# Optimization experiments

Hardware: AMD Instinct MI355X
Metric: run time of the kernel (lower is better)

## Reference

```python
import jax, jax.numpy as jnp
import numpy as np

T_STEPS = 64      # AR order p
MAX_T = 65536     # trajectory length
BATCH = 256       # number of sampled trajectories
STD = 0.3


def setup_inputs() -> dict:
    key = jax.random.key(0)
    k1, k2, k3 = jax.random.split(key, 3)
    raw = jax.random.normal(k1, (T_STEPS,), dtype=jnp.float32)
    # torch init: params / sum(|params|)
    params = raw / jnp.sum(jnp.abs(raw))
    bias = jax.random.uniform(k2, (1,), dtype=jnp.float32)
    noise = jax.random.normal(k3, (BATCH, MAX_T), dtype=jnp.float32)
    return {"params": params, "bias": bias, "noise": noise}


def _ar_means(params, bias, length):
    """AR(p) recurrence: mean_i = sum_k params[k] * x[i-1-k] + bias, x init = 0.
    State holds the last p values, most-recent-first (matches the reversed
    indexing inputs[i-1 : i-p-1 : -1] in the torch code)."""
    p = params.shape[0]

    def step(state, _):
        new = jnp.dot(state, params) + bias[0]
        state = jnp.concatenate([new[None], state[:-1]])
        return state, new

    init = jnp.zeros((p,), dtype=params.dtype)
    _, means = jax.lax.scan(step, init, None, length=length)
    return means  # [length]


def reference(params, bias, noise):
    # means of the Normal over the trajectory (deterministic, shared by batch)
    means = _ar_means(params, bias, noise.shape[1])  # [T]
    # reparameterized sample: actions = mean + std * eps, eps ~ N(0, 1)
    actions = means[None, :] + jnp.asarray(STD, noise.dtype) * noise  # [B, T]
    return actions
```

## Files before the change

kernel.cpp:

```cpp
#include <hip/hip_runtime.h>

#define T_LEN   65536
#define BATCH   256
#define P       64
#define K1_LEN  8192
#define K1_THREADS 256
#define W_TILE  1024
#define BCHUNK  8
#define VOFF    65536
#define V3OFF   (VOFF + 80)

typedef float f4 __attribute__((ext_vector_type(4)));


__global__ __launch_bounds__(K1_THREADS, 1) void ar_k1(const float* __restrict__ params,
                                                       float* __restrict__ R) {
    __shared__ __align__(16) float Rl[K1_LEN];
    __shared__ float p[128];
    __shared__ float Wp[64][4];
    __shared__ __align__(16) float Vs[68];
    __shared__ __align__(16) float tailb[192];
    __shared__ float t3[128];
    const int tid = threadIdx.x;
    if (tid < 128) p[tid] = (tid < P) ? params[tid] : 0.f;
    __syncthreads();

    if (tid < 64) {
        float z = 0.f;
        const float pk = p[tid];
        for (int t = 0; t < 64; ++t) {
            float y  = __shfl(z, 0) + 1.0f;
            float zn = __shfl_down(z, 1);
            if (tid == 63) zn = 0.f;
            z = fmaf(pk, y, zn);
            if (tid == 0) Rl[t] = y;
        }
    }
    __syncthreads();

    for (int L = 64; L <= K1_LEN; L <<= 1) {
        const bool last = (L == K1_LEN);
        {
            const int j = tid >> 2, c = tid & 3;
            const int mbase = c << 4;
            float w = 0.f;
            #pragma unroll
            for (int mm = 0; mm < 16; ++mm) {
                const int m = mbase + mm;
                w = fmaf(p[m + j], Rl[L - 1 - m], w);
            }
            Wp[j][c] = w;
        }
        __syncthreads();
        if (tid <= P) {
            const float wj  = (tid < P)
                ? (Wp[tid][0] + Wp[tid][1] + Wp[tid][2] + Wp[tid][3]) : 0.f;
            const float wm1 = (tid >= 1)
                ? (Wp[tid-1][0] + Wp[tid-1][1] + Wp[tid-1][2] + Wp[tid-1][3]) : 0.f;
            Vs[tid] = wj - wm1;
        }
        __syncthreads();
        if (tid < P) {
            const int tau = tid;
            float acc = Rl[tau];
            #pragma unroll
            for (int i = 0; i < P; ++i) {
                const int idx = (tau - i) > 0 ? (tau - i) : 0;
                const float v = (i <= tau) ? Vs[i] : 0.f;
                acc = fmaf(v, Rl[idx], acc);
            }
            if (last) R[L + tau] = acc; else Rl[L + tau] = acc;
        }
        {
            const f4* __restrict__ Rl4 = reinterpret_cast<const f4*>(Rl);
            f4* __restrict__ Rl4w = reinterpret_cast<f4*>(Rl);
            f4* __restrict__ Rg4  = reinterpret_cast<f4*>(R);
            const f4* __restrict__ V4 = reinterpret_cast<const f4*>(Vs);
            const int nq = (L - 64) >> 2;
            #pragma unroll 1
            for (int q = tid; q < nq; q += K1_THREADS) {
                f4 w4[17];
                #pragma unroll
                for (int j = 0; j < 17; ++j) w4[j] = Rl4[q + j];
                float a0 = w4[16].x, a1 = w4[16].y, a2 = w4[16].z, a3 = w4[16].w;
                #pragma unroll
                for (int g = 0; g < 16; ++g) {
                    const f4 v  = V4[g];
                    const f4 hi = w4[16 - g];
                    const f4 lo = w4[15 - g];
                    a0 = fmaf(v.x, hi.x, a0); a1 = fmaf(v.x, hi.y, a1);
                    a2 = fmaf(v.x, hi.z, a2); a3 = fmaf(v.x, hi.w, a3);
                    a0 = fmaf(v.y, lo.w, a0); a1 = fmaf(v.y, hi.x, a1);
                    a2 = fmaf(v.y, hi.y, a2); a3 = fmaf(v.y, hi.z, a3);
                    a0 = fmaf(v.z, lo.z, a0); a1 = fmaf(v.z, lo.w, a1);
                    a2 = fmaf(v.z, hi.x, a2); a3 = fmaf(v.z, hi.y, a3);
                    a0 = fmaf(v.w, lo.y, a0); a1 = fmaf(v.w, lo.z, a1);
                    a2 = fmaf(v.w, lo.w, a2); a3 = fmaf(v.w, hi.x, a3);
                }
                const float v64 = Vs[64];
                a0 = fmaf(v64, w4[0].x, a0); a1 = fmaf(v64, w4[0].y, a1);
                a2 = fmaf(v64, w4[0].z, a2); a3 = fmaf(v64, w4[0].w, a3);
                f4 o; o.x = a0; o.y = a1; o.z = a2; o.w = a3;
                if (last) {
                    Rg4[((L + 64) >> 2) + q] = o;
                    if (q >= 1984) reinterpret_cast<f4*>(tailb)[q - 1984] = o;
                } else {
                    Rl4w[((L + 64) >> 2) + q] = o;
                }
            }
        }
        __syncthreads();
    }

    {
        const int j = tid >> 2, c = tid & 3, mbase = c << 4;
        float w = 0.f;
        #pragma unroll
        for (int mm = 0; mm < 16; ++mm) {
            const int m = mbase + mm;
            w = fmaf(p[m + j], tailb[191 - m], w);
        }
        Wp[j][c] = w;
    }
    __syncthreads();
    if (tid <= P) {
        const float wj  = (tid < P)
            ? (Wp[tid][0] + Wp[tid][1] + Wp[tid][2] + Wp[tid][3]) : 0.f;
        const float wm1 = (tid >= 1)
            ? (Wp[tid-1][0] + Wp[tid-1][1] + Wp[tid-1][2] + Wp[tid-1][3]) : 0.f;
        const float v = wj - wm1;
        Vs[tid] = v;
        R[VOFF + tid] = v;
    }
    __syncthreads();
    if (tid < 128) {
        float acc = tailb[64 + tid];
        #pragma unroll
        for (int i = 0; i <= P; ++i)
            acc = fmaf(Vs[i], tailb[64 + tid - i], acc);
        t3[tid] = acc;
    }
    __syncthreads();
    {
        const int j = tid >> 2, c = tid & 3, mbase = c << 4;
        float w = 0.f;
        #pragma unroll
        for (int mm = 0; mm < 16; ++mm) {
            const int m = mbase + mm;
            w = fmaf(p[m + j], t3[127 - m], w);
        }
        Wp[j][c] = w;
    }
    __syncthreads();
    if (tid <= P) {
        const float wj  = (tid < P)
            ? (Wp[tid][0] + Wp[tid][1] + Wp[tid][2] + Wp[tid][3]) : 0.f;
        const float wm1 = (tid >= 1)
            ? (Wp[tid-1][0] + Wp[tid-1][1] + Wp[tid-1][2] + Wp[tid-1][3]) : 0.f;
        R[V3OFF + tid] = wj - wm1;
    }

    for (int j = tid; j < K1_LEN / 4; j += K1_THREADS)
        reinterpret_cast<f4*>(R)[j] = reinterpret_cast<const f4*>(Rl)[j];
}

__global__ __launch_bounds__(256) void ar_out_fused(const float* __restrict__ R,
                                                    const float* __restrict__ bias,
                                                    const float* __restrict__ noise,
                                                    float* __restrict__ out) {
    __shared__ __align__(16) float Rt[W_TILE];
    __shared__ float winA[W_TILE + 64];
    __shared__ float winB[W_TILE + 128];
    __shared__ float V2l[72], V3l[72];
    const int tid  = threadIdx.x;
    const int tile = blockIdx.x & 63;
    const int bc   = blockIdx.x >> 6;
    const int t0   = tile * W_TILE;
    const float b  = bias[0];

    if (tid < 65)       V2l[tid] = R[VOFF + tid];
    else if (tid < 130) V3l[tid - 65] = R[V3OFF + (tid - 65)];

    f4 rt;
    if (t0 < 16384) {
        const f4 r = reinterpret_cast<const f4*>(R)[(t0 >> 2) + tid];
        rt.x = b * r.x; rt.y = b * r.y; rt.z = b * r.z; rt.w = b * r.w;
    } else if (t0 < 32768) {
        const int u0 = t0 - 16384;
        for (int k = tid; k < W_TILE + 64; k += 256) {
            const int u = u0 - 64 + k;
            winA[k] = (u >= 0) ? R[u] : 0.f;
        }
        __syncthreads();
        for (int j = tid; j < W_TILE; j += 256) {
            float acc = winA[64 + j];
            #pragma unroll
            for (int i = 0; i <= P; ++i)
                acc = fmaf(V2l[i], winA[64 + j - i], acc);
            Rt[j] = b * acc;
        }
        __syncthreads();
        rt = reinterpret_cast<const f4*>(Rt)[tid];
    } else {
        const int tau0 = t0 - 32768;
        const int s0   = tau0 - 64;
        if (tau0 >= 16384) {
            const int wb0 = s0 - 16448;
            for (int k = tid; k < W_TILE + 128; k += 256) {
                const int u = wb0 + k;
                winB[k] = (u >= 0) ? R[u] : 0.f;
            }
        }
        __syncthreads();
        for (int k = tid; k < W_TILE + 64; k += 256) {
            const int u = s0 + k;
            float v;
            if (u < 0) {
                v = 0.f;
            } else if (u < 16384) {
                v = R[u];
            } else {
                float a = winB[k + 64];
                #pragma unroll
                for (int i = 0; i <= P; ++i)
                    a = fmaf(V2l[i], winB[k + 64 - i], a);
                v = a;
            }
            winA[k] = v;
        }
        __syncthreads();
        for (int j = tid; j < W_TILE; j += 256) {
            float acc = winA[64 + j];
            #pragma unroll
            for (int i = 0; i <= P; ++i)
                acc = fmaf(V3l[i], winA[64 + j - i], acc);
            Rt[j] = b * acc;
        }
        __syncthreads();
        rt = reinterpret_cast<const f4*>(Rt)[tid];
    }

    const int nb4 = T_LEN >> 2;
    const int col = (t0 >> 2) + tid;
    const f4* __restrict__ n4 = reinterpret_cast<const f4*>(noise);
    f4* __restrict__ o4 = reinterpret_cast<f4*>(out);
    #pragma unroll
    for (int bi = 0; bi < BCHUNK; ++bi) {
        const int idx = (bc * BCHUNK + bi) * nb4 + col;
        const f4 n = __builtin_nontemporal_load(n4 + idx);
        f4 o;
        o.x = fmaf(0.3f, n.x, rt.x);
        o.y = fmaf(0.3f, n.y, rt.y);
        o.z = fmaf(0.3f, n.z, rt.z);
        o.w = fmaf(0.3f, n.w, rt.w);
        __builtin_nontemporal_store(o, o4 + idx);
    }
}

extern "C" void kernel_launch(void* const* d_in, const int* in_sizes, int n_in,
                              void* d_out, int out_size, void* d_ws, size_t ws_size,
                              hipStream_t stream) {
    const float* params = (const float*)d_in[0];
    const float* bias   = (const float*)d_in[1];
    const float* noise  = (const float*)d_in[2];
    float* out = (float*)d_out;
    float* R   = (float*)d_ws;

    hipLaunchKernelGGL(ar_k1, dim3(1), dim3(K1_THREADS), 0, stream, params, R);
    hipLaunchKernelGGL(ar_out_fused, dim3(64 * 32), dim3(256), 0, stream,
                       R, bias, noise, out);
}
```

Baseline: 168.7 us.

## Shrink serial base to 4096 and derive per-segment transfer kernels via doubling schedule

The serial first kernel now builds only a 4096-length impulse response instead of 8192. It then runs a fixed 14-step schedule that composes 65-tap correction kernels for each of the 16 segments of length 4096, using small 256-wide tails. The output kernel now does one 65-tap convolution per tile from the base response, with register-blocked f4 FMAs, instead of the two-level nested convolution it used for later tiles. This shortens the single-block serial phase and evens out per-tile work, at the cost of extra schedule steps with barriers in the first kernel.

```diff
diff --git a/kernel.cpp b/kernel.cpp
--- a/kernel.cpp
+++ b/kernel.cpp
@@ -3,24 +3,29 @@
 #define T_LEN   65536
 #define BATCH   256
 #define P       64
-#define K1_LEN  8192
+#define BASE    4096
 #define K1_THREADS 256
 #define W_TILE  1024
 #define BCHUNK  8
 #define VOFF    65536
-#define V3OFF   (VOFF + 80)
 
 typedef float f4 __attribute__((ext_vector_type(4)));
 
+
+__constant__ int SCH_DST[14] = { 2, 3, 4, 6, 5, 7, 8,10,12,14, 9,11,13,15};
+__constant__ int SCH_SRC[14] = { 1, 2, 2, 3, 4, 6, 4, 5, 6, 7, 8,10,12,14};
+__constant__ int SCH_DBL[14] = { 1, 0, 1, 1, 0, 0, 1, 1, 1, 1, 0, 0, 0, 0};
+__constant__ int SCH_W[14]   = {192,256,128,192,256,256,64,192,128,192,256,256,256,256};
 
 __global__ __launch_bounds__(K1_THREADS, 1) void ar_k1(const float* __restrict__ params,
                                                        float* __restrict__ R) {
-    __shared__ __align__(16) float Rl[K1_LEN];
+    __shared__ __align__(16) float Rl[BASE];
     __shared__ float p[128];
     __shared__ float Wp[64][4];
     __shared__ __align__(16) float Vs[68];
-    __shared__ __align__(16) float tailb[192];
-    __shared__ float t3[128];
+    __shared__ __align__(16) float Vnode[16][68];
+    __shared__ __align__(16) float Tn[8][256];
+    __shared__ __align__(16) float Ts[256];
     const int tid = threadIdx.x;
     if (tid < 128) p[tid] = (tid < P) ? params[tid] : 0.f;
     __syncthreads();
@@ -38,8 +43,7 @@
     }
     __syncthreads();
 
-    for (int L = 64; L <= K1_LEN; L <<= 1) {
-        const bool last = (L == K1_LEN);
+    for (int L = 64; L <= BASE / 2; L <<= 1) {
         {
             const int j = tid >> 2, c = tid & 3;
             const int mbase = c << 4;
@@ -69,12 +73,11 @@
                 const float v = (i <= tau) ? Vs[i] : 0.f;
                 acc = fmaf(v, Rl[idx], acc);
             }
-            if (last) R[L + tau] = acc; else Rl[L + tau] = acc;
+            Rl[L + tau] = acc;
         }
         {
             const f4* __restrict__ Rl4 = reinterpret_cast<const f4*>(Rl);
             f4* __restrict__ Rl4w = reinterpret_cast<f4*>(Rl);
-            f4* __restrict__ Rg4  = reinterpret_cast<f4*>(R);
             const f4* __restrict__ V4 = reinterpret_cast<const f4*>(Vs);
             const int nq = (L - 64) >> 2;
             #pragma unroll 1
@@ -101,24 +104,24 @@
                 a0 = fmaf(v64, w4[0].x, a0); a1 = fmaf(v64, w4[0].y, a1);
                 a2 = fmaf(v64, w4[0].z, a2); a3 = fmaf(v64, w4[0].w, a3);
                 f4 o; o.x = a0; o.y = a1; o.z = a2; o.w = a3;
-                if (last) {
-                    Rg4[((L + 64) >> 2) + q] = o;
-                    if (q >= 1984) reinterpret_cast<f4*>(tailb)[q - 1984] = o;
-                } else {
-                    Rl4w[((L + 64) >> 2) + q] = o;
-                }
-            }
-        }
-        __syncthreads();
-    }
-
+                Rl4w[((L + 64) >> 2) + q] = o;
+            }
+        }
+        __syncthreads();
+    }
+
+    for (int j = tid; j < BASE / 4; j += K1_THREADS)
+        reinterpret_cast<f4*>(R)[j] = reinterpret_cast<const f4*>(Rl)[j];
+
+    Tn[1][tid] = Rl[3840 + tid];
+    __syncthreads();
     {
         const int j = tid >> 2, c = tid & 3, mbase = c << 4;
         float w = 0.f;
         #pragma unroll
         for (int mm = 0; mm < 16; ++mm) {
             const int m = mbase + mm;
-            w = fmaf(p[m + j], tailb[191 - m], w);
+            w = fmaf(p[m + j], Tn[1][255 - m], w);
         }
         Wp[j][c] = w;
     }
@@ -128,116 +131,105 @@
             ? (Wp[tid][0] + Wp[tid][1] + Wp[tid][2] + Wp[tid][3]) : 0.f;
         const float wm1 = (tid >= 1)
             ? (Wp[tid-1][0] + Wp[tid-1][1] + Wp[tid-1][2] + Wp[tid-1][3]) : 0.f;
-        const float v = wj - wm1;
-        Vs[tid] = v;
-        R[VOFF + tid] = v;
-    }
-    __syncthreads();
-    if (tid < 128) {
-        float acc = tailb[64 + tid];
-        #pragma unroll
-        for (int i = 0; i <= P; ++i)
-            acc = fmaf(Vs[i], tailb[64 + tid - i], acc);
-        t3[tid] = acc;
-    }
-    __syncthreads();
-    {
-        const int j = tid >> 2, c = tid & 3, mbase = c << 4;
-        float w = 0.f;
-        #pragma unroll
-        for (int mm = 0; mm < 16; ++mm) {
-            const int m = mbase + mm;
-            w = fmaf(p[m + j], t3[127 - m], w);
-        }
-        Wp[j][c] = w;
-    }
-    __syncthreads();
-    if (tid <= P) {
-        const float wj  = (tid < P)
-            ? (Wp[tid][0] + Wp[tid][1] + Wp[tid][2] + Wp[tid][3]) : 0.f;
-        const float wm1 = (tid >= 1)
-            ? (Wp[tid-1][0] + Wp[tid-1][1] + Wp[tid-1][2] + Wp[tid-1][3]) : 0.f;
-        R[V3OFF + tid] = wj - wm1;
-    }
-
-    for (int j = tid; j < K1_LEN / 4; j += K1_THREADS)
-        reinterpret_cast<f4*>(R)[j] = reinterpret_cast<const f4*>(Rl)[j];
+        Vnode[1][tid] = wj - wm1;
+    }
+    __syncthreads();
+
+    for (int s = 0; s < 14; ++s) {
+        const int dst = SCH_DST[s], src = SCH_SRC[s], wd = SCH_W[s];
+        const bool dbl = SCH_DBL[s] != 0;
+        float* td = (dst <= 7) ? Tn[dst] : Ts;
+        const float* tsrc = Tn[src];
+        const float* Vsr  = Vnode[src];
+        if (tid < wd) {
+            const float* s0 = dbl ? (tsrc + 64) : (Rl + 3840);
+            float acc = s0[tid];
+            #pragma unroll
+            for (int i = 0; i <= P; ++i)
+                acc = fmaf(Vsr[i], s0[tid - i], acc);
+            td[tid] = acc;
+        }
+        __syncthreads();
+        {
+            const int j = tid >> 2, c = tid & 3, mbase = c << 4;
+            float w = 0.f;
+            #pragma unroll
+            for (int mm = 0; mm < 16; ++mm) {
+                const int m = mbase + mm;
+                w = fmaf(p[m + j], td[wd - 1 - m], w);
+            }
+            Wp[j][c] = w;
+        }
+        __syncthreads();
+        if (tid <= P) {
+            const float wj  = (tid < P)
+                ? (Wp[tid][0] + Wp[tid][1] + Wp[tid][2] + Wp[tid][3]) : 0.f;
+            const float wm1 = (tid >= 1)
+                ? (Wp[tid-1][0] + Wp[tid-1][1] + Wp[tid-1][2] + Wp[tid-1][3]) : 0.f;
+            Vnode[dst][tid] = wj - wm1;
+        }
+        __syncthreads();
+    }
+
+    for (int j = tid; j < 15 * 80; j += K1_THREADS) {
+        const int k = j / 80 + 1, i = j - (k - 1) * 80;
+        if (i < 65) R[VOFF + k * 80 + i] = Vnode[k][i];
+    }
 }
 
 __global__ __launch_bounds__(256) void ar_out_fused(const float* __restrict__ R,
                                                     const float* __restrict__ bias,
                                                     const float* __restrict__ noise,
                                                     float* __restrict__ out) {
-    __shared__ __align__(16) float Rt[W_TILE];
-    __shared__ float winA[W_TILE + 64];
-    __shared__ float winB[W_TILE + 128];
-    __shared__ float V2l[72], V3l[72];
+    __shared__ __align__(16) float win[1088];
+    __shared__ __align__(16) float Vl[68];
     const int tid  = threadIdx.x;
     const int tile = blockIdx.x & 63;
     const int bc   = blockIdx.x >> 6;
     const int t0   = tile * W_TILE;
     const float b  = bias[0];
-
-    if (tid < 65)       V2l[tid] = R[VOFF + tid];
-    else if (tid < 130) V3l[tid - 65] = R[V3OFF + (tid - 65)];
+    const int k    = t0 >> 12;
+    const f4* __restrict__ Rg4 = reinterpret_cast<const f4*>(R);
 
     f4 rt;
-    if (t0 < 16384) {
-        const f4 r = reinterpret_cast<const f4*>(R)[(t0 >> 2) + tid];
+    if (k == 0) {
+        const f4 r = Rg4[(t0 >> 2) + tid];
         rt.x = b * r.x; rt.y = b * r.y; rt.z = b * r.z; rt.w = b * r.w;
-    } else if (t0 < 32768) {
-        const int u0 = t0 - 16384;
-        for (int k = tid; k < W_TILE + 64; k += 256) {
-            const int u = u0 - 64 + k;
-            winA[k] = (u >= 0) ? R[u] : 0.f;
-        }
-        __syncthreads();
-        for (int j = tid; j < W_TILE; j += 256) {
-            float acc = winA[64 + j];
-            #pragma unroll
-            for (int i = 0; i <= P; ++i)
-                acc = fmaf(V2l[i], winA[64 + j - i], acc);
-            Rt[j] = b * acc;
-        }
-        __syncthreads();
-        rt = reinterpret_cast<const f4*>(Rt)[tid];
     } else {
-        const int tau0 = t0 - 32768;
-        const int s0   = tau0 - 64;
-        if (tau0 >= 16384) {
-            const int wb0 = s0 - 16448;
-            for (int k = tid; k < W_TILE + 128; k += 256) {
-                const int u = wb0 + k;
-                winB[k] = (u >= 0) ? R[u] : 0.f;
-            }
-        }
-        __syncthreads();
-        for (int k = tid; k < W_TILE + 64; k += 256) {
-            const int u = s0 + k;
-            float v;
-            if (u < 0) {
-                v = 0.f;
-            } else if (u < 16384) {
-                v = R[u];
-            } else {
-                float a = winB[k + 64];
-                #pragma unroll
-                for (int i = 0; i <= P; ++i)
-                    a = fmaf(V2l[i], winB[k + 64 - i], a);
-                v = a;
-            }
-            winA[k] = v;
-        }
-        __syncthreads();
-        for (int j = tid; j < W_TILE; j += 256) {
-            float acc = winA[64 + j];
-            #pragma unroll
-            for (int i = 0; i <= P; ++i)
-                acc = fmaf(V3l[i], winA[64 + j - i], acc);
-            Rt[j] = b * acc;
-        }
-        __syncthreads();
-        rt = reinterpret_cast<const f4*>(Rt)[tid];
+        const int tau0 = t0 & 4095;
+        if (tid < 65) Vl[tid] = R[VOFF + k * 80 + tid];
+        f4* __restrict__ win4 = reinterpret_cast<f4*>(win);
+        for (int j4 = tid; j4 < 272; j4 += 256) {
+            const int u = tau0 - 64 + 4 * j4;
+            f4 v;
+            if (u >= 0) v = Rg4[u >> 2];
+            else { v.x = 0.f; v.y = 0.f; v.z = 0.f; v.w = 0.f; }
+            win4[j4] = v;
+        }
+        __syncthreads();
+        const f4* __restrict__ V4 = reinterpret_cast<const f4*>(Vl);
+        f4 w4[17];
+        #pragma unroll
+        for (int j = 0; j < 17; ++j) w4[j] = win4[tid + j];
+        float a0 = w4[16].x, a1 = w4[16].y, a2 = w4[16].z, a3 = w4[16].w;
+        #pragma unroll
+        for (int g = 0; g < 16; ++g) {
+            const f4 v  = V4[g];
+            const f4 hi = w4[16 - g];
+            const f4 lo = w4[15 - g];
+            a0 = fmaf(v.x, hi.x, a0); a1 = fmaf(v.x, hi.y, a1);
+            a2 = fmaf(v.x, hi.z, a2); a3 = fmaf(v.x, hi.w, a3);
+            a0 = fmaf(v.y, lo.w, a0); a1 = fmaf(v.y, hi.x, a1);
+            a2 = fmaf(v.y, hi.y, a2); a3 = fmaf(v.y, hi.z, a3);
+            a0 = fmaf(v.z, lo.z, a0); a1 = fmaf(v.z, lo.w, a1);
+            a2 = fmaf(v.z, hi.x, a2); a3 = fmaf(v.z, hi.y, a3);
+            a0 = fmaf(v.w, lo.y, a0); a1 = fmaf(v.w, lo.z, a1);
+            a2 = fmaf(v.w, lo.w, a2); a3 = fmaf(v.w, hi.x, a3);
+        }
+        const float v64 = Vl[64];
+        a0 = fmaf(v64, w4[0].x, a0); a1 = fmaf(v64, w4[0].y, a1);
+        a2 = fmaf(v64, w4[0].z, a2); a3 = fmaf(v64, w4[0].w, a3);
+        rt.x = b * a0; rt.y = b * a1; rt.z = b * a2; rt.w = b * a3;
     }
 
     const int nb4 = T_LEN >> 2;
```

Result: no change. 166.3 us (-1.4%).
